# Kernel optimization log

Hardware: AMD Instinct MI355X
Metric: run time of the kernel (lower is better)

The kernel has to match this reference:

```python
import jax, jax.numpy as jnp
import numpy as np

N, L, H, E, FE = 32, 128, 16, 256, 4  # batch, seq_len, heads, embed_size, forward_expansion
EPS = 1e-5
NEG_SLOPE = 0.01


def _mask_positions(qe):
    # zero entries where j < L-1-i (torch: triu(ones,1).flip(1) == 1)
    Ld = qe.shape[-1]
    i = jnp.arange(Ld)[:, None]
    j = jnp.arange(Ld)[None, :]
    return jnp.where(j >= (Ld - 1 - i), qe, jnp.zeros((), qe.dtype))


def _skew(qe):
    # pad last dim on the left, reinterpret, drop first row -> relative skew
    n, h, Ld, _ = qe.shape
    p = jnp.pad(qe, ((0, 0), (0, 0), (0, 0), (1, 0)))
    return p.reshape(n, h, Ld + 1, Ld)[:, :, 1:, :]


def _batchnorm(x, gamma, beta):
    # BatchNorm1d(C=L*H) over (N, C, E): normalize over batch and embed dims
    mean = jnp.mean(x, axis=(0, 2), keepdims=True)
    var = jnp.var(x, axis=(0, 2), keepdims=True)
    return (x - mean) * jax.lax.rsqrt(var + EPS) * gamma[None, :, None] + beta[None, :, None]


def _leaky(x):
    return jnp.where(x >= 0, x, NEG_SLOPE * x)


def setup_inputs() -> dict:
    key = jax.random.key(0)
    ks = jax.random.split(key, 16)
    s_e = 1.0 / np.sqrt(E)
    d = {
        "x": jax.random.normal(ks[0], (N, L * H, E, 1), dtype=jnp.float32),
        "Wq": jax.random.normal(ks[1], (E, E), dtype=jnp.float32) * s_e,
        "bq": jnp.zeros((E,), jnp.float32),
        "Wk": jax.random.normal(ks[2], (E, E), dtype=jnp.float32) * s_e,
        "bk": jnp.zeros((E,), jnp.float32),
        "Wv": jax.random.normal(ks[3], (E, E), dtype=jnp.float32) * s_e,
        "bv": jnp.zeros((E,), jnp.float32),
        "Erel": jax.random.normal(ks[4], (H, L, E), dtype=jnp.float32),
        "Wo": jax.random.normal(ks[5], (E, E), dtype=jnp.float32) * s_e,
        "bo": jnp.zeros((E,), jnp.float32),
        "g1": jnp.ones((L * H,), jnp.float32),
        "be1": jnp.zeros((L * H,), jnp.float32),
        "g2": jnp.ones((L * H,), jnp.float32),
        "be2": jnp.zeros((L * H,), jnp.float32),
        "W1": jax.random.normal(ks[6], (E, FE * E), dtype=jnp.float32) * s_e,
        "b1": jnp.zeros((FE * E,), jnp.float32),
        "W2": jax.random.normal(ks[7], (FE * E, E), dtype=jnp.float32) * (1.0 / np.sqrt(FE * E)),
        "b2": jnp.zeros((E,), jnp.float32),
        "Wenc": jax.random.normal(ks[8], (E, E), dtype=jnp.float32) * s_e,
        "benc": jnp.zeros((E,), jnp.float32),
    }
    return d


def reference(x, Wq, bq, Wk, bk, Wv, bv, Erel, Wo, bo, g1, be1, g2, be2, W1, b1, W2, b2, Wenc, benc):
    xs = x[:, :, :, 0]  # (N, L*H, E)
    q = (xs @ Wq + bq).reshape(N, L, H, E)
    k = (xs @ Wk + bk).reshape(N, L, H, E)
    v = (xs @ Wv + bv).reshape(N, L, H, E)
    # relative-position skew term (Music-Transformer style)
    QE = jnp.einsum('nlhe,hme->nhlm', q, Erel)       # (N,H,L,L)
    S = _skew(_mask_positions(QE))                   # (N,H,L,L)
    qk = jnp.einsum('nqhe,nkhe->nhqk', q, k)         # (N,H,L,L)
    att = jax.nn.softmax(qk / jnp.sqrt(jnp.float32(E)), axis=-1) + S
    z = jnp.einsum('nhql,nlhe->nqhe', att, v).reshape(N, L * H, E)
    z = z @ Wo + bo
    h1 = _batchnorm(z + xs, g1, be1)
    ff = _leaky(h1 @ W1 + b1) @ W2 + b2
    out = _batchnorm(ff + h1, g2, be2)
    return out @ Wenc + benc
```

## Files before the change

kernel.cpp:

```cpp
#include <hip/hip_runtime.h>
#include <hip/hip_bf16.h>

using u16 = unsigned short;
typedef __attribute__((ext_vector_type(8))) short bf16x8;
typedef __attribute__((ext_vector_type(4))) float f32x4;

static constexpr float EPS_ = 1e-5f;
static constexpr float NEG_ = 0.01f;

__device__ __forceinline__ float bf2f(u16 u) { return __uint_as_float(((unsigned)u) << 16); }
__device__ __forceinline__ u16 f2bf(float f) {
    union { __hip_bfloat16 h; u16 u; } c; c.h = __float2bfloat16(f); return c.u;
}

#define MFMA16(a, b, c) __builtin_amdgcn_mfma_f32_16x16x32_bf16(a, b, c, 0, 0, 0)

__device__ __forceinline__ void gload16(const u16* g, u16* l) {
    __builtin_amdgcn_global_load_lds(
        (__attribute__((address_space(1))) void*)(u16*)g,
        (__attribute__((address_space(3))) void*)l, 16, 0, 0);
}

__device__ __forceinline__ int xswz(int nwg) {
    const int b = blockIdx.x;
    return (b & 7) * (nwg >> 3) + (b >> 3);
}

template<int K>
__device__ __forceinline__ void core256(
    const u16* __restrict__ Ag, int lda,
    const u16* __restrict__ Bg, int ldb,
    u16* SH, f32x4 acc[8][4])
{
    const int tid = threadIdx.x;
    const int w = tid >> 6, lane = tid & 63;
    const int g = lane >> 4, r = lane & 15;
    const int wr = w >> 2, wc = w & 3;
    const int gx = (g ^ ((r >> 1) & 3)) * 8;
    constexpr int NT = K / 32;

    #pragma unroll
    for (int i = 0; i < 8; i++)
        #pragma unroll
        for (int j = 0; j < 4; j++)
            acc[i][j] = (f32x4){0.f, 0.f, 0.f, 0.f};

    auto stage = [&](int buf, int kt, int rnd) {
        const int part = rnd & 1, isB = rnd >> 1;
        const int u = part * 512 + tid;
        const int row = u >> 2;
        const int sc = (u & 3) ^ ((row >> 1) & 3);
        const u16* src = (isB ? Bg + (size_t)row * ldb : Ag + (size_t)row * lda)
                         + kt + sc * 8;
        gload16(src, SH + buf * 16384 + isB * 8192 + u * 8);
    };

    #pragma unroll
    for (int rnd = 0; rnd < 4; ++rnd) stage(0, 0, rnd);
    #pragma unroll
    for (int rnd = 0; rnd < 4; ++rnd) stage(1, 32, rnd);
    asm volatile("s_waitcnt vmcnt(4)" ::: "memory");
    __builtin_amdgcn_s_barrier();
    __builtin_amdgcn_sched_barrier(0);

    int cur = 0;
    for (int t = 0; t < NT; ++t) {
        const u16* Ab = SH + cur * 16384;
        const u16* Bb = Ab + 8192;
        const bool pf = (t + 2 < NT);
        const int nb = cur + 2 >= 3 ? cur - 1 : cur + 2;

        if (pf) { stage(nb, (t + 2) * 32, 0); stage(nb, (t + 2) * 32, 1); }
        bf16x8 bfr[4], af[4];
        #pragma unroll
        for (int fn = 0; fn < 4; ++fn)
            bfr[fn] = *(const bf16x8*)(Bb + (wc * 64 + fn * 16 + r) * 32 + gx);
        #pragma unroll
        for (int f = 0; f < 4; ++f)
            af[f] = *(const bf16x8*)(Ab + (wr * 128 + f * 16 + r) * 32 + gx);
        __builtin_amdgcn_s_setprio(1);
        #pragma unroll
        for (int f = 0; f < 4; ++f)
            #pragma unroll
            for (int fn = 0; fn < 4; ++fn)
                acc[f][fn] = MFMA16(af[f], bfr[fn], acc[f][fn]);
        __builtin_amdgcn_s_setprio(0);

        if (pf) { stage(nb, (t + 2) * 32, 2); stage(nb, (t + 2) * 32, 3); }
        #pragma unroll
        for (int f = 0; f < 4; ++f)
            af[f] = *(const bf16x8*)(Ab + (wr * 128 + 64 + f * 16 + r) * 32 + gx);
        __builtin_amdgcn_s_setprio(1);
        #pragma unroll
        for (int f = 0; f < 4; ++f)
            #pragma unroll
            for (int fn = 0; fn < 4; ++fn)
                acc[4 + f][fn] = MFMA16(af[f], bfr[fn], acc[4 + f][fn]);
        __builtin_amdgcn_s_setprio(0);

        if (pf) asm volatile("s_waitcnt vmcnt(4)" ::: "memory");
        else    asm volatile("s_waitcnt vmcnt(0)" ::: "memory");
        __builtin_amdgcn_s_barrier();
        __builtin_amdgcn_sched_barrier(0);
        cur = cur + 1 == 3 ? 0 : cur + 1;
    }
}

template<int K, int NN, int MODE>
__global__ __launch_bounds__(512, 2) void gemm256_k(
    const u16* __restrict__ A, const u16* __restrict__ Bt,
    const float* __restrict__ bias, const u16* __restrict__ res,
    const float2* __restrict__ rp, const float* __restrict__ cs,
    void* __restrict__ outv)
{
    __shared__ __align__(16) u16 SH[49152];
    constexpr int NB = NN / 256;
    const int f = xswz(256 * NB);
    const int m0 = (f / NB) * 256, n0 = (f % NB) * 256;

    f32x4 acc[8][4];
    core256<K>(A + (size_t)m0 * K, K, Bt + (size_t)n0 * K, K, SH, acc);

    const int tid = threadIdx.x;
    const int w = tid >> 6, lane = tid & 63;
    const int g = lane >> 4, r = lane & 15;
    const int wr = w >> 2, wc = w & 3;

    if constexpr (MODE == 3) {
        float* out = (float*)outv;
        #pragma unroll
        for (int fn = 0; fn < 4; ++fn) {
            const int n = n0 + wc * 64 + fn * 16 + r;
            const float bv = bias[n], cv = cs[n];
            #pragma unroll
            for (int fm = 0; fm < 8; ++fm)
                #pragma unroll
                for (int reg = 0; reg < 4; ++reg) {
                    const int m = m0 + wr * 128 + fm * 16 + g * 4 + reg;
                    const float2 pp = rp[m & 2047];
                    out[(size_t)m * NN + n] = pp.x * acc[fm][fn][reg] + pp.y * cv + bv;
                }
        }
        return;
    }
    __syncthreads();
    u16* out = (u16*)outv;
    #pragma unroll
    for (int h = 0; h < 2; ++h) {
        if (wr == h) {
            #pragma unroll
            for (int fm = 0; fm < 8; ++fm)
                #pragma unroll
                for (int fn = 0; fn < 4; ++fn) {
                    const int col = wc * 64 + fn * 16 + r;
                    const float bv = bias[n0 + col];
                    #pragma unroll
                    for (int reg = 0; reg < 4; ++reg) {
                        const int rl = fm * 16 + g * 4 + reg;
                        float v = acc[fm][fn][reg];
                        if constexpr (MODE == 1) {
                            const float2 pp = rp[(m0 + h * 128 + rl) & 2047];
                            v = pp.x * v + pp.y * cs[n0 + col] + bv;
                            v = v >= 0.f ? v : NEG_ * v;
                        } else {
                            v += bv;
                        }
                        SH[rl * 264 + col] = f2bf(v);
                    }
                }
        }
        __builtin_amdgcn_s_barrier();
        #pragma unroll
        for (int p = 0; p < 8; ++p) {
            const int ck = p * 512 + tid;
            const int rl = ck >> 5, cc = ck & 31;
            const int m = m0 + h * 128 + rl;
            bf16x8 v = *(const bf16x8*)(SH + rl * 264 + cc * 8);
            if constexpr (MODE == 0) {
                const bf16x8 rv = *(const bf16x8*)(res + (size_t)m * NN + n0 + cc * 8);
                #pragma unroll
                for (int j = 0; j < 8; ++j)
                    v[j] = (short)f2bf(bf2f((u16)v[j]) + bf2f((u16)rv[j]));
            }
            if constexpr (MODE == 2) {
                const float2 pp = rp[m & 2047];
                const bf16x8 rv = *(const bf16x8*)(res + (size_t)m * NN + n0 + cc * 8);
                #pragma unroll
                for (int j = 0; j < 8; ++j)
                    v[j] = (short)f2bf(bf2f((u16)v[j]) + pp.x * bf2f((u16)rv[j]) + pp.y);
            }
            *(bf16x8*)(out + (size_t)m * NN + n0 + cc * 8) = v;
        }
        __builtin_amdgcn_s_barrier();
    }
}

__global__ __launch_bounds__(512, 2) void qkv256_k(
    const u16* __restrict__ xbf, const u16* __restrict__ Wqkvt,
    const float* __restrict__ bq, const float* __restrict__ bk,
    const float* __restrict__ bv,
    u16* __restrict__ qo, u16* __restrict__ ko, u16* __restrict__ vo)
{
    __shared__ __align__(16) u16 SH[49152];
    const int f = xswz(768);
    const int m0 = (f / 3) * 256;
    const int which = f % 3;
    const float* bias = which == 0 ? bq : (which == 1 ? bk : bv);

    f32x4 acc[8][4];
    core256<256>(xbf + (size_t)m0 * 256, 256,
                 Wqkvt + (size_t)which * 65536, 256, SH, acc);

    const int tid = threadIdx.x;
    const int w = tid >> 6, lane = tid & 63;
    const int g = lane >> 4, r = lane & 15;
    const int wr = w >> 2, wc = w & 3;
    const int nn = m0 >> 11;

    __syncthreads();
    if (which < 2) {
        u16* out = which == 0 ? qo : ko;
        #pragma unroll
        for (int h = 0; h < 2; ++h) {
            if (wr == h) {
                #pragma unroll
                for (int fm = 0; fm < 8; ++fm)
                    #pragma unroll
                    for (int fn = 0; fn < 4; ++fn) {
                        const int col = wc * 64 + fn * 16 + r;
                        const float bv4 = bias[col];
                        #pragma unroll
                        for (int reg = 0; reg < 4; ++reg) {
                            const int rl = fm * 16 + g * 4 + reg;
                            SH[rl * 264 + col] = f2bf(acc[fm][fn][reg] + bv4);
                        }
                    }
            }
            __builtin_amdgcn_s_barrier();
            #pragma unroll
            for (int p = 0; p < 8; ++p) {
                const int ck = p * 512 + tid;
                const int rl = ck >> 5, cc = ck & 31;
                const int m = m0 + h * 128 + rl;
                const int l = (m & 2047) >> 4, hh = m & 15;
                const bf16x8 v = *(const bf16x8*)(SH + rl * 264 + cc * 8);
                *(bf16x8*)(out + ((size_t)(nn * 16 + hh) * 128 + l) * 256 + cc * 8) = v;
            }
            __builtin_amdgcn_s_barrier();
        }
    } else {
        #pragma unroll
        for (int h = 0; h < 2; ++h) {
            if (wr == h) {
                #pragma unroll
                for (int fm = 0; fm < 8; ++fm)
                    #pragma unroll
                    for (int fn = 0; fn < 4; ++fn) {
                        const int col = wc * 64 + fn * 16 + r;
                        const float bv4 = bias[col];
                        #pragma unroll
                        for (int reg = 0; reg < 4; ++reg) {
                            const int rl = fm * 16 + g * 4 + reg;
                            SH[col * 136 + ((rl & 15) * 8 | (rl >> 4))] =
                                f2bf(acc[fm][fn][reg] + bv4);
                        }
                    }
            }
            __builtin_amdgcn_s_barrier();
            const int l0 = ((m0 + h * 128) & 2047) >> 4;
            #pragma unroll
            for (int p = 0; p < 8; ++p) {
                const int ck = p * 512 + tid;
                const int e = ck >> 4, hh = ck & 15;
                const bf16x8 v = *(const bf16x8*)(SH + e * 136 + hh * 8);
                *(bf16x8*)(vo + ((size_t)(nn * 16 + hh) * 256 + e) * 128 + l0) = v;
            }
            __builtin_amdgcn_s_barrier();
        }
    }
}

__device__ __forceinline__ void lds_core(
    const u16* __restrict__ Ag, int lda,
    const u16* __restrict__ Bg, int ldb, int K,
    u16* As, u16* Bs, f32x4 acc[4][4])
{
    const int tid = threadIdx.x;
    const int w = tid >> 6, lane = tid & 63;
    const int g = lane >> 4, r = lane & 15;
    const int wm = (w >> 1) * 64, wn = (w & 1) * 64;
    const int rx = r & 7;

    for (int kt = 0; kt < K; kt += 64) {
        #pragma unroll
        for (int j = 0; j < 4; j++) {
            const int ubase = (w * 4 + j) * 64;
            const int u = ubase + lane;
            const int row = u >> 3;
            const int cb = ((u & 7) ^ (row & 7)) * 8;
            gload16(Ag + (size_t)row * lda + kt + cb, As + ubase * 8);
            gload16(Bg + (size_t)row * ldb + kt + cb, Bs + ubase * 8);
        }
        __syncthreads();
        #pragma unroll
        for (int kk = 0; kk < 2; kk++) {
            const int co = ((kk * 4 + g) ^ rx) * 8;
            bf16x8 af[4], bfr[4];
            #pragma unroll
            for (int f = 0; f < 4; f++) {
                af[f]  = *(const bf16x8*)(As + (wm + f * 16 + r) * 64 + co);
                bfr[f] = *(const bf16x8*)(Bs + (wn + f * 16 + r) * 64 + co);
            }
            #pragma unroll
            for (int i = 0; i < 4; i++)
                #pragma unroll
                for (int j = 0; j < 4; j++)
                    acc[i][j] = MFMA16(af[i], bfr[j], acc[i][j]);
        }
        __syncthreads();
    }
}

template<typename OutF>
__device__ __forceinline__ void epi_store128(
    u16* Cs, f32x4 (&acc)[4][4], float scale, OutF outp)
{
    const int tid = threadIdx.x;
    const int w = tid >> 6, lane = tid & 63;
    const int g = lane >> 4, r = lane & 15;
    const int mb = (w >> 1) * 64, nb = (w & 1) * 64;

    #pragma unroll
    for (int fn = 0; fn < 4; fn++) {
        const int col = nb + fn * 16 + r;
        #pragma unroll
        for (int fm = 0; fm < 4; fm++)
            #pragma unroll
            for (int reg = 0; reg < 4; reg++) {
                const int row = mb + fm * 16 + g * 4 + reg;
                Cs[row * 136 + col] = f2bf(acc[fm][fn][reg] * scale);
            }
    }
    __syncthreads();
    #pragma unroll
    for (int p = 0; p < 8; p++) {
        const int ck = p * 256 + tid;
        const int row = ck >> 4, cc = ck & 15;
        const bf16x8 v = *(const bf16x8*)(Cs + row * 136 + cc * 8);
        *(bf16x8*)outp(row, cc) = v;
    }
}

__global__ __launch_bounds__(256) void qkqe_k(
    const u16* __restrict__ q, const u16* __restrict__ kc,
    const u16* __restrict__ erel, u16* __restrict__ out)
{
    __shared__ __align__(16) u16 SH[17408];
    u16* As = SH; u16* Bs = SH + 8192;
    const int f = xswz(1024);
    const int b = f >> 1, h = b & 15;
    const int n0 = (f & 1) * 128;
    const u16* Ag = q + (size_t)b * 128 * 256;
    const u16* Bg = (n0 == 0) ? (kc + (size_t)b * 128 * 256)
                              : (erel + (size_t)h * 128 * 256);

    f32x4 acc[4][4];
    #pragma unroll
    for (int i = 0; i < 4; i++)
        #pragma unroll
        for (int j = 0; j < 4; j++) acc[i][j] = (f32x4){0.f,0.f,0.f,0.f};
    lds_core(Ag, 256, Bg, 256, 256, As, Bs, acc);

    const float scale = (n0 == 0) ? 0.0625f : 1.0f;
    __syncthreads();
    epi_store128(SH, acc, scale,
        [&](int row, int cc) -> u16* {
            return out + ((size_t)b * 128 + row) * 256 + n0 + cc * 8;
        });
}

__global__ __launch_bounds__(256) void softmax_k(
    const u16* __restrict__ qk, u16* __restrict__ att)
{
    const int r = blockIdx.x * 4 + (threadIdx.x >> 6);
    const int lane = threadIdx.x & 63;
    const int i = r & 127;
    const u16* row = qk + (size_t)r * 256;
    const float x0 = bf2f(row[lane]), x1 = bf2f(row[lane + 64]);
    float mx = fmaxf(x0, x1);
    #pragma unroll
    for (int o = 32; o; o >>= 1) mx = fmaxf(mx, __shfl_xor(mx, o));
    const float e0 = __expf(x0 - mx), e1 = __expf(x1 - mx);
    float s = e0 + e1;
    #pragma unroll
    for (int o = 32; o; o >>= 1) s += __shfl_xor(s, o);
    const float rinv = 1.0f / s;
    const float s0 = (lane <= i) ? bf2f(row[128 + 127 - i + lane]) : 0.f;
    const float s1 = (lane + 64 <= i) ? bf2f(row[128 + 127 - i + lane + 64]) : 0.f;
    att[(size_t)r * 128 + lane] = f2bf(e0 * rinv + s0);
    att[(size_t)r * 128 + lane + 64] = f2bf(e1 * rinv + s1);
}

__global__ __launch_bounds__(256) void av_k(
    const u16* __restrict__ att, const u16* __restrict__ vT,
    u16* __restrict__ zc)
{
    __shared__ __align__(16) u16 SH[17408];
    u16* As = SH; u16* Bs = SH + 8192;
    const int f = xswz(1024);
    const int b = f >> 1;
    const int n0 = (f & 1) * 128;
    const u16* Ag = att + (size_t)b * 128 * 128;
    const u16* Bg = vT + (size_t)b * 256 * 128 + (size_t)n0 * 128;

    f32x4 acc[4][4];
    #pragma unroll
    for (int i = 0; i < 4; i++)
        #pragma unroll
        for (int j = 0; j < 4; j++) acc[i][j] = (f32x4){0.f,0.f,0.f,0.f};
    lds_core(Ag, 128, Bg, 128, 128, As, Bs, acc);

    const int nn = b >> 4, hh = b & 15;
    __syncthreads();
    epi_store128(SH, acc, 1.f,
        [&](int row, int cc) -> u16* {
            return zc + ((size_t)(nn * 2048 + row * 16 + hh)) * 256 + n0 + cc * 8;
        });
}

__global__ __launch_bounds__(256) void cvt_k(const float* __restrict__ in,
                                             u16* __restrict__ out) {
    const size_t i8 = ((size_t)blockIdx.x * 256 + threadIdx.x) * 8;
    const float4 lo = *(const float4*)(in + i8);
    const float4 hi = *(const float4*)(in + i8 + 4);
    ushort4 o0, o1;
    o0.x = f2bf(lo.x); o0.y = f2bf(lo.y); o0.z = f2bf(lo.z); o0.w = f2bf(lo.w);
    o1.x = f2bf(hi.x); o1.y = f2bf(hi.y); o1.z = f2bf(hi.z); o1.w = f2bf(hi.w);
    *(ushort4*)(out + i8) = o0;
    *(ushort4*)(out + i8 + 4) = o1;
}

__global__ __launch_bounds__(256) void prep_w_k(
    const float* __restrict__ Wq, const float* __restrict__ Wk,
    const float* __restrict__ Wv, const float* __restrict__ Wo,
    const float* __restrict__ Wenc, const float* __restrict__ W1,
    const float* __restrict__ W2, const float* __restrict__ Erel,
    u16* __restrict__ Wqkvt, u16* __restrict__ Wot, u16* __restrict__ Wenct,
    u16* __restrict__ W1t, u16* __restrict__ W2t, u16* __restrict__ Erelb,
    float* __restrict__ cs1, float* __restrict__ csE)
{
    const int bid = blockIdx.x, tid = threadIdx.x;
    if (bid < 1280) {
        const int jb = bid >> 8;
        const int t = ((bid & 255) << 8) | tid;
        const int n = t >> 8, k = t & 255;
        const float* src = jb == 0 ? Wq : jb == 1 ? Wk : jb == 2 ? Wv
                         : jb == 3 ? Wo : Wenc;
        const u16 v = f2bf(src[(k << 8) + n]);
        if (jb < 3)       Wqkvt[jb * 65536 + t] = v;
        else if (jb == 3) Wot[t] = v;
        else              Wenct[t] = v;
    } else if (bid < 2304) {
        const int t = ((bid - 1280) << 8) | tid;
        const int n = t >> 8, k = t & 255;
        W1t[t] = f2bf(W1[(k << 10) + n]);
    } else if (bid < 3328) {
        const int t = ((bid - 2304) << 8) | tid;
        const int n = t >> 10, k = t & 1023;
        W2t[t] = f2bf(W2[(k << 8) + n]);
    } else if (bid < 5376) {
        const int t = ((bid - 3328) << 8) | tid;
        Erelb[t] = f2bf(Erel[t]);
    } else {
        const int n = (bid - 5376) * 256 + tid;
        if (n < 1024) {
            float s = 0.f;
            for (int k = 0; k < 256; ++k) s += bf2f(f2bf(W1[(size_t)k * 1024 + n]));
            cs1[n] = s;
        } else {
            const int n2 = n - 1024;
            float s = 0.f;
            for (int k = 0; k < 256; ++k) s += bf2f(f2bf(Wenc[(size_t)k * 256 + n2]));
            csE[n2] = s;
        }
    }
}

__global__ __launch_bounds__(256) void bnstats_k(
    const u16* __restrict__ x, const float* __restrict__ g,
    const float* __restrict__ be, float2* __restrict__ params)
{
    const int c = blockIdx.x, tid = threadIdx.x;
    float s = 0.f, s2 = 0.f;
    #pragma unroll 4
    for (int n = 0; n < 32; n++) {
        const float v = bf2f(x[((size_t)n * 2048 + c) * 256 + tid]);
        s += v; s2 += v * v;
    }
    #pragma unroll
    for (int o = 32; o; o >>= 1) { s += __shfl_xor(s, o); s2 += __shfl_xor(s2, o); }
    __shared__ float rs[4], rs2[4];
    const int w = tid >> 6;
    if ((tid & 63) == 0) { rs[w] = s; rs2[w] = s2; }
    __syncthreads();
    if (tid == 0) {
        s  = rs[0] + rs[1] + rs[2] + rs[3];
        s2 = rs2[0] + rs2[1] + rs2[2] + rs2[3];
        const float mean = s / 8192.f;
        const float var = s2 / 8192.f - mean * mean;
        const float a = g[c] * rsqrtf(var + EPS_);
        params[c] = make_float2(a, be[c] - mean * a);
    }
}

extern "C" void kernel_launch(void* const* d_in, const int* in_sizes, int n_in,
                              void* d_out, int out_size, void* d_ws, size_t ws_size,
                              hipStream_t stream)
{
    const float* x    = (const float*)d_in[0];
    const float* Wq   = (const float*)d_in[1];
    const float* bq   = (const float*)d_in[2];
    const float* Wk   = (const float*)d_in[3];
    const float* bk   = (const float*)d_in[4];
    const float* Wv   = (const float*)d_in[5];
    const float* bv   = (const float*)d_in[6];
    const float* Erel = (const float*)d_in[7];
    const float* Wo   = (const float*)d_in[8];
    const float* bo   = (const float*)d_in[9];
    const float* g1   = (const float*)d_in[10];
    const float* be1  = (const float*)d_in[11];
    const float* g2   = (const float*)d_in[12];
    const float* be2  = (const float*)d_in[13];
    const float* W1   = (const float*)d_in[14];
    const float* b1   = (const float*)d_in[15];
    const float* W2   = (const float*)d_in[16];
    const float* b2   = (const float*)d_in[17];
    const float* Wenc = (const float*)d_in[18];
    const float* benc = (const float*)d_in[19];

    char* ws = (char*)d_ws;
    const size_t MB = 1ull << 20;
    const size_t KB = 1024;
    u16* xbf   = (u16*)(ws + 0 * MB);
    u16* h2pre = (u16*)(ws + 32 * MB);
    u16* qb    = (u16*)(ws + 32 * MB);
    u16* kb    = (u16*)(ws + 64 * MB);
    u16* vT    = (u16*)(ws + 96 * MB);
    u16* qkb   = (u16*)(ws + 128 * MB);
    u16* attb  = (u16*)(ws + 160 * MB);
    u16* ff1   = (u16*)(ws + 64 * MB);
    u16* zc    = (u16*)(ws + 176 * MB);
    u16* h1pre = (u16*)(ws + 208 * MB);
    u16* Wqkvt = (u16*)(ws + 240 * MB);
    u16* Wot   = (u16*)(ws + 240 * MB + 512 * KB);
    u16* Wenct = (u16*)(ws + 240 * MB + 640 * KB);
    u16* W1t   = (u16*)(ws + 240 * MB + 768 * KB);
    u16* W2t   = (u16*)(ws + 240 * MB + 1280 * KB);
    u16* Erelb = (u16*)(ws + 240 * MB + 1792 * KB);
    float2* p1 = (float2*)(ws + 243 * MB);
    float2* p2 = (float2*)(ws + 243 * MB + 16 * KB);
    float* cs1 = (float*)(ws + 243 * MB + 32 * KB);
    float* csE = (float*)(ws + 243 * MB + 40 * KB);

    const dim3 b256(256), b512(512);

    cvt_k<<<dim3(8192), b256, 0, stream>>>(x, xbf);
    prep_w_k<<<dim3(5381), b256, 0, stream>>>(Wq, Wk, Wv, Wo, Wenc, W1, W2, Erel,
                                              Wqkvt, Wot, Wenct, W1t, W2t, Erelb,
                                              cs1, csE);

    qkv256_k<<<dim3(768), b512, 0, stream>>>(xbf, Wqkvt, bq, bk, bv, qb, kb, vT);
    qkqe_k<<<dim3(1024), b256, 0, stream>>>(qb, kb, Erelb, qkb);
    softmax_k<<<dim3(16384), b256, 0, stream>>>(qkb, attb);
    av_k<<<dim3(1024), b256, 0, stream>>>(attb, vT, zc);
    gemm256_k<256, 256, 0><<<dim3(256), b512, 0, stream>>>(
        zc, Wot, bo, xbf, nullptr, nullptr, h1pre);

    bnstats_k<<<dim3(2048), b256, 0, stream>>>(h1pre, g1, be1, p1);

    gemm256_k<256, 1024, 1><<<dim3(1024), b512, 0, stream>>>(
        h1pre, W1t, b1, nullptr, p1, cs1, ff1);
    gemm256_k<1024, 256, 2><<<dim3(256), b512, 0, stream>>>(
        ff1, W2t, b2, h1pre, p1, nullptr, h2pre);

    bnstats_k<<<dim3(2048), b256, 0, stream>>>(h2pre, g2, be2, p2);
    gemm256_k<256, 256, 3><<<dim3(256), b512, 0, stream>>>(
        h2pre, Wenct, benc, nullptr, p2, csE, (float*)d_out);
}
```

Before: 349.4 us.

## Switch GEMM core to double buffering, raise occupancy, stage fp32 output through LDS

The shared GEMM core goes from a three-deep to a two-deep LDS pipeline with a full vmcnt(0) wait each iteration. This shrinks shared memory to 72KB so launch bounds can ask for 4 blocks per CU instead of 2. The fp32 final-projection epilogue now writes results into LDS in 64-row chunks and then stores them as coalesced float4 rows, instead of scattered scalar stores. The trade-off is less prefetch depth and tighter waits, plus register pressure from the higher occupancy target (128 VGPRs with 512 threads), which may cause spills given the 128 accumulator floats per thread.

```diff
diff --git a/kernel.cpp b/kernel.cpp
--- a/kernel.cpp
+++ b/kernel.cpp
@@ -57,20 +57,17 @@
 
     #pragma unroll
     for (int rnd = 0; rnd < 4; ++rnd) stage(0, 0, rnd);
-    #pragma unroll
-    for (int rnd = 0; rnd < 4; ++rnd) stage(1, 32, rnd);
-    asm volatile("s_waitcnt vmcnt(4)" ::: "memory");
+    asm volatile("s_waitcnt vmcnt(0)" ::: "memory");
     __builtin_amdgcn_s_barrier();
     __builtin_amdgcn_sched_barrier(0);
 
-    int cur = 0;
     for (int t = 0; t < NT; ++t) {
-        const u16* Ab = SH + cur * 16384;
+        const int buf = t & 1;
+        const u16* Ab = SH + buf * 16384;
         const u16* Bb = Ab + 8192;
-        const bool pf = (t + 2 < NT);
-        const int nb = cur + 2 >= 3 ? cur - 1 : cur + 2;
-
-        if (pf) { stage(nb, (t + 2) * 32, 0); stage(nb, (t + 2) * 32, 1); }
+        const bool pf = (t + 1 < NT);
+
+        if (pf) { stage(buf ^ 1, (t + 1) * 32, 0); stage(buf ^ 1, (t + 1) * 32, 1); }
         bf16x8 bfr[4], af[4];
         #pragma unroll
         for (int fn = 0; fn < 4; ++fn)
@@ -86,7 +83,7 @@
                 acc[f][fn] = MFMA16(af[f], bfr[fn], acc[f][fn]);
         __builtin_amdgcn_s_setprio(0);
 
-        if (pf) { stage(nb, (t + 2) * 32, 2); stage(nb, (t + 2) * 32, 3); }
+        if (pf) { stage(buf ^ 1, (t + 1) * 32, 2); stage(buf ^ 1, (t + 1) * 32, 3); }
         #pragma unroll
         for (int f = 0; f < 4; ++f)
             af[f] = *(const bf16x8*)(Ab + (wr * 128 + 64 + f * 16 + r) * 32 + gx);
@@ -98,22 +95,20 @@
                 acc[4 + f][fn] = MFMA16(af[f], bfr[fn], acc[4 + f][fn]);
         __builtin_amdgcn_s_setprio(0);
 
-        if (pf) asm volatile("s_waitcnt vmcnt(4)" ::: "memory");
-        else    asm volatile("s_waitcnt vmcnt(0)" ::: "memory");
+        asm volatile("s_waitcnt vmcnt(0)" ::: "memory");
         __builtin_amdgcn_s_barrier();
         __builtin_amdgcn_sched_barrier(0);
-        cur = cur + 1 == 3 ? 0 : cur + 1;
     }
 }
 
 template<int K, int NN, int MODE>
-__global__ __launch_bounds__(512, 2) void gemm256_k(
+__global__ __launch_bounds__(512, 4) void gemm256_k(
     const u16* __restrict__ A, const u16* __restrict__ Bt,
     const float* __restrict__ bias, const u16* __restrict__ res,
     const float2* __restrict__ rp, const float* __restrict__ cs,
     void* __restrict__ outv)
 {
-    __shared__ __align__(16) u16 SH[49152];
+    __shared__ __align__(16) u16 SH[36864];
     constexpr int NB = NN / 256;
     const int f = xswz(256 * NB);
     const int m0 = (f / NB) * 256, n0 = (f % NB) * 256;
@@ -126,24 +121,45 @@
     const int g = lane >> 4, r = lane & 15;
     const int wr = w >> 2, wc = w & 3;
 
+    __syncthreads();
+
     if constexpr (MODE == 3) {
+        float* SHf = (float*)SH;
         float* out = (float*)outv;
         #pragma unroll
-        for (int fn = 0; fn < 4; ++fn) {
-            const int n = n0 + wc * 64 + fn * 16 + r;
-            const float bv = bias[n], cv = cs[n];
-            #pragma unroll
-            for (int fm = 0; fm < 8; ++fm)
+        for (int q = 0; q < 4; ++q) {
+            if (wr == (q >> 1)) {
+                const int fmB = (q & 1) * 4;
                 #pragma unroll
-                for (int reg = 0; reg < 4; ++reg) {
-                    const int m = m0 + wr * 128 + fm * 16 + g * 4 + reg;
-                    const float2 pp = rp[m & 2047];
-                    out[(size_t)m * NN + n] = pp.x * acc[fm][fn][reg] + pp.y * cv + bv;
+                for (int fi = 0; fi < 4; ++fi) {
+                    #pragma unroll
+                    for (int fn = 0; fn < 4; ++fn) {
+                        const int col = wc * 64 + fn * 16 + r;
+                        const float bv = bias[n0 + col], cv = cs[n0 + col];
+                        #pragma unroll
+                        for (int reg = 0; reg < 4; ++reg) {
+                            const int rl = fi * 16 + g * 4 + reg;
+                            const int m = m0 + q * 64 + rl;
+                            const float2 pp = rp[m & 2047];
+                            SHf[rl * 260 + col] =
+                                pp.x * acc[fmB + fi][fn][reg] + pp.y * cv + bv;
+                        }
+                    }
                 }
+            }
+            __builtin_amdgcn_s_barrier();
+            #pragma unroll
+            for (int p = 0; p < 8; ++p) {
+                const int id = p * 512 + tid;
+                const int rl = id >> 6, c4 = id & 63;
+                const float4 v = *(const float4*)(SHf + rl * 260 + c4 * 4);
+                *(float4*)(out + (size_t)(m0 + q * 64 + rl) * 256 + c4 * 4) = v;
+            }
+            __builtin_amdgcn_s_barrier();
         }
         return;
     }
-    __syncthreads();
+
     u16* out = (u16*)outv;
     #pragma unroll
     for (int h = 0; h < 2; ++h) {
@@ -195,13 +211,13 @@
     }
 }
 
-__global__ __launch_bounds__(512, 2) void qkv256_k(
+__global__ __launch_bounds__(512, 4) void qkv256_k(
     const u16* __restrict__ xbf, const u16* __restrict__ Wqkvt,
     const float* __restrict__ bq, const float* __restrict__ bk,
     const float* __restrict__ bv,
     u16* __restrict__ qo, u16* __restrict__ ko, u16* __restrict__ vo)
 {
-    __shared__ __align__(16) u16 SH[49152];
+    __shared__ __align__(16) u16 SH[36864];
     const int f = xswz(768);
     const int m0 = (f / 3) * 256;
     const int which = f % 3;
```

After: 1.168 ms. +234.4%, slower.

## Replace 256x256 triple-buffered GEMM tiles with 128x128 lds_core tiles

Applied to the files above, without the earlier changes.

Removes the 512-thread 256x256 triple-buffered core256 GEMM path and routes the QKV projection and all dense GEMMs through the existing 256-thread 128x128 lds_core tile, launching four times as many workgroups. The fp32 output GEMM now stages results through LDS for coalesced float4 stores instead of scattered scalar writes. This aims for better load balance across CUs with more, smaller blocks. In exchange it gives up the larger tile's operand reuse and the explicit async global-to-LDS prefetch pipeline.

```diff
diff --git a/kernel.cpp b/kernel.cpp
--- a/kernel.cpp
+++ b/kernel.cpp
@@ -24,260 +24,6 @@
 __device__ __forceinline__ int xswz(int nwg) {
     const int b = blockIdx.x;
     return (b & 7) * (nwg >> 3) + (b >> 3);
-}
-
-template<int K>
-__device__ __forceinline__ void core256(
-    const u16* __restrict__ Ag, int lda,
-    const u16* __restrict__ Bg, int ldb,
-    u16* SH, f32x4 acc[8][4])
-{
-    const int tid = threadIdx.x;
-    const int w = tid >> 6, lane = tid & 63;
-    const int g = lane >> 4, r = lane & 15;
-    const int wr = w >> 2, wc = w & 3;
-    const int gx = (g ^ ((r >> 1) & 3)) * 8;
-    constexpr int NT = K / 32;
-
-    #pragma unroll
-    for (int i = 0; i < 8; i++)
-        #pragma unroll
-        for (int j = 0; j < 4; j++)
-            acc[i][j] = (f32x4){0.f, 0.f, 0.f, 0.f};
-
-    auto stage = [&](int buf, int kt, int rnd) {
-        const int part = rnd & 1, isB = rnd >> 1;
-        const int u = part * 512 + tid;
-        const int row = u >> 2;
-        const int sc = (u & 3) ^ ((row >> 1) & 3);
-        const u16* src = (isB ? Bg + (size_t)row * ldb : Ag + (size_t)row * lda)
-                         + kt + sc * 8;
-        gload16(src, SH + buf * 16384 + isB * 8192 + u * 8);
-    };
-
-    #pragma unroll
-    for (int rnd = 0; rnd < 4; ++rnd) stage(0, 0, rnd);
-    #pragma unroll
-    for (int rnd = 0; rnd < 4; ++rnd) stage(1, 32, rnd);
-    asm volatile("s_waitcnt vmcnt(4)" ::: "memory");
-    __builtin_amdgcn_s_barrier();
-    __builtin_amdgcn_sched_barrier(0);
-
-    int cur = 0;
-    for (int t = 0; t < NT; ++t) {
-        const u16* Ab = SH + cur * 16384;
-        const u16* Bb = Ab + 8192;
-        const bool pf = (t + 2 < NT);
-        const int nb = cur + 2 >= 3 ? cur - 1 : cur + 2;
-
-        if (pf) { stage(nb, (t + 2) * 32, 0); stage(nb, (t + 2) * 32, 1); }
-        bf16x8 bfr[4], af[4];
-        #pragma unroll
-        for (int fn = 0; fn < 4; ++fn)
-            bfr[fn] = *(const bf16x8*)(Bb + (wc * 64 + fn * 16 + r) * 32 + gx);
-        #pragma unroll
-        for (int f = 0; f < 4; ++f)
-            af[f] = *(const bf16x8*)(Ab + (wr * 128 + f * 16 + r) * 32 + gx);
-        __builtin_amdgcn_s_setprio(1);
-        #pragma unroll
-        for (int f = 0; f < 4; ++f)
-            #pragma unroll
-            for (int fn = 0; fn < 4; ++fn)
-                acc[f][fn] = MFMA16(af[f], bfr[fn], acc[f][fn]);
-        __builtin_amdgcn_s_setprio(0);
-
-        if (pf) { stage(nb, (t + 2) * 32, 2); stage(nb, (t + 2) * 32, 3); }
-        #pragma unroll
-        for (int f = 0; f < 4; ++f)
-            af[f] = *(const bf16x8*)(Ab + (wr * 128 + 64 + f * 16 + r) * 32 + gx);
-        __builtin_amdgcn_s_setprio(1);
-        #pragma unroll
-        for (int f = 0; f < 4; ++f)
-            #pragma unroll
-            for (int fn = 0; fn < 4; ++fn)
-                acc[4 + f][fn] = MFMA16(af[f], bfr[fn], acc[4 + f][fn]);
-        __builtin_amdgcn_s_setprio(0);
-
-        if (pf) asm volatile("s_waitcnt vmcnt(4)" ::: "memory");
-        else    asm volatile("s_waitcnt vmcnt(0)" ::: "memory");
-        __builtin_amdgcn_s_barrier();
-        __builtin_amdgcn_sched_barrier(0);
-        cur = cur + 1 == 3 ? 0 : cur + 1;
-    }
-}
-
-template<int K, int NN, int MODE>
-__global__ __launch_bounds__(512, 2) void gemm256_k(
-    const u16* __restrict__ A, const u16* __restrict__ Bt,
-    const float* __restrict__ bias, const u16* __restrict__ res,
-    const float2* __restrict__ rp, const float* __restrict__ cs,
-    void* __restrict__ outv)
-{
-    __shared__ __align__(16) u16 SH[49152];
-    constexpr int NB = NN / 256;
-    const int f = xswz(256 * NB);
-    const int m0 = (f / NB) * 256, n0 = (f % NB) * 256;
-
-    f32x4 acc[8][4];
-    core256<K>(A + (size_t)m0 * K, K, Bt + (size_t)n0 * K, K, SH, acc);
-
-    const int tid = threadIdx.x;
-    const int w = tid >> 6, lane = tid & 63;
-    const int g = lane >> 4, r = lane & 15;
-    const int wr = w >> 2, wc = w & 3;
-
-    if constexpr (MODE == 3) {
-        float* out = (float*)outv;
-        #pragma unroll
-        for (int fn = 0; fn < 4; ++fn) {
-            const int n = n0 + wc * 64 + fn * 16 + r;
-            const float bv = bias[n], cv = cs[n];
-            #pragma unroll
-            for (int fm = 0; fm < 8; ++fm)
-                #pragma unroll
-                for (int reg = 0; reg < 4; ++reg) {
-                    const int m = m0 + wr * 128 + fm * 16 + g * 4 + reg;
-                    const float2 pp = rp[m & 2047];
-                    out[(size_t)m * NN + n] = pp.x * acc[fm][fn][reg] + pp.y * cv + bv;
-                }
-        }
-        return;
-    }
-    __syncthreads();
-    u16* out = (u16*)outv;
-    #pragma unroll
-    for (int h = 0; h < 2; ++h) {
-        if (wr == h) {
-            #pragma unroll
-            for (int fm = 0; fm < 8; ++fm)
-                #pragma unroll
-                for (int fn = 0; fn < 4; ++fn) {
-                    const int col = wc * 64 + fn * 16 + r;
-                    const float bv = bias[n0 + col];
-                    #pragma unroll
-                    for (int reg = 0; reg < 4; ++reg) {
-                        const int rl = fm * 16 + g * 4 + reg;
-                        float v = acc[fm][fn][reg];
-                        if constexpr (MODE == 1) {
-                            const float2 pp = rp[(m0 + h * 128 + rl) & 2047];
-                            v = pp.x * v + pp.y * cs[n0 + col] + bv;
-                            v = v >= 0.f ? v : NEG_ * v;
-                        } else {
-                            v += bv;
-                        }
-                        SH[rl * 264 + col] = f2bf(v);
-                    }
-                }
-        }
-        __builtin_amdgcn_s_barrier();
-        #pragma unroll
-        for (int p = 0; p < 8; ++p) {
-            const int ck = p * 512 + tid;
-            const int rl = ck >> 5, cc = ck & 31;
-            const int m = m0 + h * 128 + rl;
-            bf16x8 v = *(const bf16x8*)(SH + rl * 264 + cc * 8);
-            if constexpr (MODE == 0) {
-                const bf16x8 rv = *(const bf16x8*)(res + (size_t)m * NN + n0 + cc * 8);
-                #pragma unroll
-                for (int j = 0; j < 8; ++j)
-                    v[j] = (short)f2bf(bf2f((u16)v[j]) + bf2f((u16)rv[j]));
-            }
-            if constexpr (MODE == 2) {
-                const float2 pp = rp[m & 2047];
-                const bf16x8 rv = *(const bf16x8*)(res + (size_t)m * NN + n0 + cc * 8);
-                #pragma unroll
-                for (int j = 0; j < 8; ++j)
-                    v[j] = (short)f2bf(bf2f((u16)v[j]) + pp.x * bf2f((u16)rv[j]) + pp.y);
-            }
-            *(bf16x8*)(out + (size_t)m * NN + n0 + cc * 8) = v;
-        }
-        __builtin_amdgcn_s_barrier();
-    }
-}
-
-__global__ __launch_bounds__(512, 2) void qkv256_k(
-    const u16* __restrict__ xbf, const u16* __restrict__ Wqkvt,
-    const float* __restrict__ bq, const float* __restrict__ bk,
-    const float* __restrict__ bv,
-    u16* __restrict__ qo, u16* __restrict__ ko, u16* __restrict__ vo)
-{
-    __shared__ __align__(16) u16 SH[49152];
-    const int f = xswz(768);
-    const int m0 = (f / 3) * 256;
-    const int which = f % 3;
-    const float* bias = which == 0 ? bq : (which == 1 ? bk : bv);
-
-    f32x4 acc[8][4];
-    core256<256>(xbf + (size_t)m0 * 256, 256,
-                 Wqkvt + (size_t)which * 65536, 256, SH, acc);
-
-    const int tid = threadIdx.x;
-    const int w = tid >> 6, lane = tid & 63;
-    const int g = lane >> 4, r = lane & 15;
-    const int wr = w >> 2, wc = w & 3;
-    const int nn = m0 >> 11;
-
-    __syncthreads();
-    if (which < 2) {
-        u16* out = which == 0 ? qo : ko;
-        #pragma unroll
-        for (int h = 0; h < 2; ++h) {
-            if (wr == h) {
-                #pragma unroll
-                for (int fm = 0; fm < 8; ++fm)
-                    #pragma unroll
-                    for (int fn = 0; fn < 4; ++fn) {
-                        const int col = wc * 64 + fn * 16 + r;
-                        const float bv4 = bias[col];
-                        #pragma unroll
-                        for (int reg = 0; reg < 4; ++reg) {
-                            const int rl = fm * 16 + g * 4 + reg;
-                            SH[rl * 264 + col] = f2bf(acc[fm][fn][reg] + bv4);
-                        }
-                    }
-            }
-            __builtin_amdgcn_s_barrier();
-            #pragma unroll
-            for (int p = 0; p < 8; ++p) {
-                const int ck = p * 512 + tid;
-                const int rl = ck >> 5, cc = ck & 31;
-                const int m = m0 + h * 128 + rl;
-                const int l = (m & 2047) >> 4, hh = m & 15;
-                const bf16x8 v = *(const bf16x8*)(SH + rl * 264 + cc * 8);
-                *(bf16x8*)(out + ((size_t)(nn * 16 + hh) * 128 + l) * 256 + cc * 8) = v;
-            }
-            __builtin_amdgcn_s_barrier();
-        }
-    } else {
-        #pragma unroll
-        for (int h = 0; h < 2; ++h) {
-            if (wr == h) {
-                #pragma unroll
-                for (int fm = 0; fm < 8; ++fm)
-                    #pragma unroll
-                    for (int fn = 0; fn < 4; ++fn) {
-                        const int col = wc * 64 + fn * 16 + r;
-                        const float bv4 = bias[col];
-                        #pragma unroll
-                        for (int reg = 0; reg < 4; ++reg) {
-                            const int rl = fm * 16 + g * 4 + reg;
-                            SH[col * 136 + ((rl & 15) * 8 | (rl >> 4))] =
-                                f2bf(acc[fm][fn][reg] + bv4);
-                        }
-                    }
-            }
-            __builtin_amdgcn_s_barrier();
-            const int l0 = ((m0 + h * 128) & 2047) >> 4;
-            #pragma unroll
-            for (int p = 0; p < 8; ++p) {
-                const int ck = p * 512 + tid;
-                const int e = ck >> 4, hh = ck & 15;
-                const bf16x8 v = *(const bf16x8*)(SH + e * 136 + hh * 8);
-                *(bf16x8*)(vo + ((size_t)(nn * 16 + hh) * 256 + e) * 128 + l0) = v;
-            }
-            __builtin_amdgcn_s_barrier();
-        }
-    }
 }
 
 __device__ __forceinline__ void lds_core(
@@ -318,6 +64,195 @@
                     acc[i][j] = MFMA16(af[i], bfr[j], acc[i][j]);
         }
         __syncthreads();
+    }
+}
+
+__device__ __forceinline__ void zero4(f32x4 acc[4][4]) {
+    #pragma unroll
+    for (int i = 0; i < 4; i++)
+        #pragma unroll
+        for (int j = 0; j < 4; j++)
+            acc[i][j] = (f32x4){0.f, 0.f, 0.f, 0.f};
+}
+
+template<int K, int NN, int MODE>
+__global__ __launch_bounds__(256) void gemm128_k(
+    const u16* __restrict__ A, const u16* __restrict__ Bt,
+    const float* __restrict__ bias, const u16* __restrict__ res,
+    const float2* __restrict__ rp, const float* __restrict__ cs,
+    void* __restrict__ outv)
+{
+    __shared__ __align__(16) u16 SH[17408];
+    u16* As = SH; u16* Bs = SH + 8192;
+    constexpr int NB = NN / 128;
+    const int f = xswz(512 * NB);
+    const int m0 = (f / NB) * 128, n0 = (f % NB) * 128;
+
+    f32x4 acc[4][4]; zero4(acc);
+    lds_core(A + (size_t)m0 * K, K, Bt + (size_t)n0 * K, K, K, As, Bs, acc);
+
+    const int tid = threadIdx.x;
+    const int w = tid >> 6, lane = tid & 63;
+    const int g = lane >> 4, r = lane & 15;
+    const int mb = (w >> 1) * 64, nb = (w & 1) * 64;
+
+    __syncthreads();
+
+    if constexpr (MODE == 3) {
+        float* SHf = (float*)SH;
+        float* out = (float*)outv;
+        #pragma unroll
+        for (int q = 0; q < 4; ++q) {
+            if ((w >> 1) == (q >> 1)) {
+                const int fmB = (q & 1) * 2;
+                #pragma unroll
+                for (int fi = 0; fi < 2; ++fi) {
+                    #pragma unroll
+                    for (int fn = 0; fn < 4; ++fn) {
+                        const int col = nb + fn * 16 + r;
+                        const float bv = bias[n0 + col], cv = cs[n0 + col];
+                        #pragma unroll
+                        for (int reg = 0; reg < 4; ++reg) {
+                            const int rl = fi * 16 + g * 4 + reg;
+                            const int m = m0 + q * 32 + rl;
+                            const float2 pp = rp[m & 2047];
+                            SHf[rl * 132 + col] =
+                                pp.x * acc[fmB + fi][fn][reg] + pp.y * cv + bv;
+                        }
+                    }
+                }
+            }
+            __syncthreads();
+            #pragma unroll
+            for (int p = 0; p < 4; ++p) {
+                const int id = p * 256 + tid;
+                const int rl = id >> 5, c4 = id & 31;
+                const float4 v = *(const float4*)(SHf + rl * 132 + c4 * 4);
+                *(float4*)(out + (size_t)(m0 + q * 32 + rl) * 256 + n0 + c4 * 4) = v;
+            }
+            __syncthreads();
+        }
+        return;
+    }
+
+    u16* out = (u16*)outv;
+    #pragma unroll
+    for (int fn = 0; fn < 4; ++fn) {
+        const int col = nb + fn * 16 + r;
+        const float bv = bias[n0 + col];
+        #pragma unroll
+        for (int fm = 0; fm < 4; ++fm) {
+            #pragma unroll
+            for (int reg = 0; reg < 4; ++reg) {
+                const int rowt = mb + fm * 16 + g * 4 + reg;
+                float v = acc[fm][fn][reg];
+                if constexpr (MODE == 1) {
+                    const float2 pp = rp[(m0 + rowt) & 2047];
+                    v = pp.x * v + pp.y * cs[n0 + col] + bv;
+                    v = v >= 0.f ? v : NEG_ * v;
+                } else {
+                    v += bv;
+                }
+                SH[rowt * 136 + col] = f2bf(v);
+            }
+        }
+    }
+    __syncthreads();
+    #pragma unroll
+    for (int p = 0; p < 8; ++p) {
+        const int ck = p * 256 + tid;
+        const int rowt = ck >> 4, cc = ck & 15;
+        const int m = m0 + rowt;
+        bf16x8 v = *(const bf16x8*)(SH + rowt * 136 + cc * 8);
+        if constexpr (MODE == 0) {
+            const bf16x8 rv = *(const bf16x8*)(res + (size_t)m * NN + n0 + cc * 8);
+            #pragma unroll
+            for (int j = 0; j < 8; ++j)
+                v[j] = (short)f2bf(bf2f((u16)v[j]) + bf2f((u16)rv[j]));
+        }
+        if constexpr (MODE == 2) {
+            const float2 pp = rp[m & 2047];
+            const bf16x8 rv = *(const bf16x8*)(res + (size_t)m * NN + n0 + cc * 8);
+            #pragma unroll
+            for (int j = 0; j < 8; ++j)
+                v[j] = (short)f2bf(bf2f((u16)v[j]) + pp.x * bf2f((u16)rv[j]) + pp.y);
+        }
+        *(bf16x8*)(out + (size_t)m * NN + n0 + cc * 8) = v;
+    }
+}
+
+__global__ __launch_bounds__(256) void qkv_k(
+    const u16* __restrict__ xbf, const u16* __restrict__ Wqkvt,
+    const float* __restrict__ bq, const float* __restrict__ bk,
+    const float* __restrict__ bv,
+    u16* __restrict__ qo, u16* __restrict__ ko, u16* __restrict__ vo)
+{
+    __shared__ __align__(16) u16 SH[17408];
+    u16* As = SH; u16* Bs = SH + 8192;
+    const int f = xswz(3072);
+    const int nblk = f % 6, mblk = f / 6;
+    const int m0 = mblk * 128, n0 = nblk * 128;
+    const int which = n0 >> 8;
+    const float* bias = which == 0 ? bq : (which == 1 ? bk : bv);
+    const int e0 = n0 & 255;
+
+    f32x4 acc[4][4]; zero4(acc);
+    lds_core(xbf + (size_t)m0 * 256, 256, Wqkvt + (size_t)n0 * 256, 256, 256,
+             As, Bs, acc);
+
+    const int tid = threadIdx.x;
+    const int w = tid >> 6, lane = tid & 63;
+    const int g = lane >> 4, r = lane & 15;
+    const int mb = (w >> 1) * 64, nb = (w & 1) * 64;
+    const int nn = m0 >> 11, l0 = (m0 & 2047) >> 4;
+
+    __syncthreads();
+    if (which == 2) {
+        #pragma unroll
+        for (int fn = 0; fn < 4; ++fn) {
+            const int col = nb + fn * 16 + r;
+            const float bv4 = bias[e0 + col];
+            #pragma unroll
+            for (int fm = 0; fm < 4; ++fm)
+                #pragma unroll
+                for (int reg = 0; reg < 4; ++reg) {
+                    const int rowt = mb + fm * 16 + g * 4 + reg;
+                    SH[col * 136 + (((rowt & 15) << 3) | (rowt >> 4))] =
+                        f2bf(acc[fm][fn][reg] + bv4);
+                }
+        }
+        __syncthreads();
+        #pragma unroll
+        for (int p = 0; p < 8; ++p) {
+            const int ck = p * 256 + tid;
+            const int e = ck >> 4, hh = ck & 15;
+            const bf16x8 v = *(const bf16x8*)(SH + e * 136 + hh * 8);
+            *(bf16x8*)(vo + ((size_t)(nn * 16 + hh) * 256 + e0 + e) * 128 + l0) = v;
+        }
+    } else {
+        u16* out = which == 0 ? qo : ko;
+        #pragma unroll
+        for (int fn = 0; fn < 4; ++fn) {
+            const int col = nb + fn * 16 + r;
+            const float bv4 = bias[e0 + col];
+            #pragma unroll
+            for (int fm = 0; fm < 4; ++fm)
+                #pragma unroll
+                for (int reg = 0; reg < 4; ++reg) {
+                    const int rowt = mb + fm * 16 + g * 4 + reg;
+                    SH[rowt * 136 + col] = f2bf(acc[fm][fn][reg] + bv4);
+                }
+        }
+        __syncthreads();
+        #pragma unroll
+        for (int p = 0; p < 8; ++p) {
+            const int ck = p * 256 + tid;
+            const int rowt = ck >> 4, cc = ck & 15;
+            const int m = m0 + rowt;
+            const int l = (m & 2047) >> 4, hh = m & 15;
+            const bf16x8 v = *(const bf16x8*)(SH + rowt * 136 + cc * 8);
+            *(bf16x8*)(out + ((size_t)(nn * 16 + hh) * 128 + l) * 256 + e0 + cc * 8) = v;
+        }
     }
 }
 
@@ -364,11 +299,7 @@
     const u16* Bg = (n0 == 0) ? (kc + (size_t)b * 128 * 256)
                               : (erel + (size_t)h * 128 * 256);
 
-    f32x4 acc[4][4];
-    #pragma unroll
-    for (int i = 0; i < 4; i++)
-        #pragma unroll
-        for (int j = 0; j < 4; j++) acc[i][j] = (f32x4){0.f,0.f,0.f,0.f};
+    f32x4 acc[4][4]; zero4(acc);
     lds_core(Ag, 256, Bg, 256, 256, As, Bs, acc);
 
     const float scale = (n0 == 0) ? 0.0625f : 1.0f;
@@ -413,11 +344,7 @@
     const u16* Ag = att + (size_t)b * 128 * 128;
     const u16* Bg = vT + (size_t)b * 256 * 128 + (size_t)n0 * 128;
 
-    f32x4 acc[4][4];
-    #pragma unroll
-    for (int i = 0; i < 4; i++)
-        #pragma unroll
-        for (int j = 0; j < 4; j++) acc[i][j] = (f32x4){0.f,0.f,0.f,0.f};
+    f32x4 acc[4][4]; zero4(acc);
     lds_core(Ag, 128, Bg, 128, 128, As, Bs, acc);
 
     const int nn = b >> 4, hh = b & 15;
@@ -562,28 +489,28 @@
     float* cs1 = (float*)(ws + 243 * MB + 32 * KB);
     float* csE = (float*)(ws + 243 * MB + 40 * KB);
 
-    const dim3 b256(256), b512(512);
+    const dim3 b256(256);
 
     cvt_k<<<dim3(8192), b256, 0, stream>>>(x, xbf);
     prep_w_k<<<dim3(5381), b256, 0, stream>>>(Wq, Wk, Wv, Wo, Wenc, W1, W2, Erel,
                                               Wqkvt, Wot, Wenct, W1t, W2t, Erelb,
                                               cs1, csE);
 
-    qkv256_k<<<dim3(768), b512, 0, stream>>>(xbf, Wqkvt, bq, bk, bv, qb, kb, vT);
+    qkv_k<<<dim3(3072), b256, 0, stream>>>(xbf, Wqkvt, bq, bk, bv, qb, kb, vT);
     qkqe_k<<<dim3(1024), b256, 0, stream>>>(qb, kb, Erelb, qkb);
     softmax_k<<<dim3(16384), b256, 0, stream>>>(qkb, attb);
     av_k<<<dim3(1024), b256, 0, stream>>>(attb, vT, zc);
-    gemm256_k<256, 256, 0><<<dim3(256), b512, 0, stream>>>(
+    gemm128_k<256, 256, 0><<<dim3(1024), b256, 0, stream>>>(
         zc, Wot, bo, xbf, nullptr, nullptr, h1pre);
 
     bnstats_k<<<dim3(2048), b256, 0, stream>>>(h1pre, g1, be1, p1);
 
-    gemm256_k<256, 1024, 1><<<dim3(1024), b512, 0, stream>>>(
+    gemm128_k<256, 1024, 1><<<dim3(4096), b256, 0, stream>>>(
         h1pre, W1t, b1, nullptr, p1, cs1, ff1);
-    gemm256_k<1024, 256, 2><<<dim3(256), b512, 0, stream>>>(
+    gemm128_k<1024, 256, 2><<<dim3(1024), b256, 0, stream>>>(
         ff1, W2t, b2, h1pre, p1, nullptr, h2pre);
 
     bnstats_k<<<dim3(2048), b256, 0, stream>>>(h2pre, g2, be2, p2);
-    gemm256_k<256, 256, 3><<<dim3(256), b512, 0, stream>>>(
+    gemm128_k<256, 256, 3><<<dim3(1024), b256, 0, stream>>>(
         h2pre, Wenct, benc, nullptr, p2, csE, (float*)d_out);
 }
```

Measured after the change: 330.9 us. 1.06x faster.
